# Performance work log

Measured on AMD Instinct MI355X. Metric: run time of the kernel, lower is better.

The kernel has to match this reference:

```python
import jax, jax.numpy as jnp
import numpy as np
from jax import lax

B, N, K = 8, 4096, 64
RATIO1, R1 = 0.5, 0.2
RATIO2, R2 = 0.25, 0.4
SA1_DIMS = [3, 32, 32, 64]
SA2_DIMS = [64 + 3, 64, 64, 128]
SA3_DIMS = [128 + 3, 128, 256, 512]


def _mlp_params(key, dims, prefix):
    params = {}
    for i, (din, dout) in enumerate(zip(dims[:-1], dims[1:])):
        key, k1 = jax.random.split(key)
        s = 1.0 / np.sqrt(din)
        params[f"{prefix}_w{i}"] = jax.random.uniform(k1, (din, dout), jnp.float32, -s, s)
        params[f"{prefix}_b{i}"] = jnp.zeros((dout,), jnp.float32)
    return params, key


def setup_inputs() -> dict:
    key = jax.random.key(0)
    key, kp = jax.random.split(key)
    inp = {"pos": jax.random.uniform(kp, (B, N, 3), jnp.float32)}  # unit-cube point clouds
    p1, key = _mlp_params(key, SA1_DIMS, "sa1"); inp.update(p1)
    p2, key = _mlp_params(key, SA2_DIMS, "sa2"); inp.update(p2)
    p3, key = _mlp_params(key, SA3_DIMS, "sa3"); inp.update(p3)
    key, k1, k2 = jax.random.split(key, 3)
    s = 1.0 / np.sqrt(512)
    inp["w_mu"] = jax.random.uniform(k1, (512, 32), jnp.float32, -s, s)
    inp["b_mu"] = jnp.zeros((32,), jnp.float32)
    inp["w_lv"] = jax.random.uniform(k2, (512, 32), jnp.float32, -s, s)
    inp["b_lv"] = jnp.zeros((32,), jnp.float32)
    return inp


def _mlp(x, params):
    # PyG MLP semantics (plain_last=True): ReLU on all but the final layer.
    for i, (w, b) in enumerate(params):
        x = x @ w + b
        if i < len(params) - 1:
            x = jax.nn.relu(x)
    return x


def _fps(pos, M):
    # Farthest point sampling, deterministic start at index 0. pos: [N,3] -> [M]
    n = pos.shape[0]
    def step(carry, _):
        dist, far = carry
        d = jnp.sum((pos - pos[far]) ** 2, axis=-1)
        dist = jnp.minimum(dist, d)
        return (dist, jnp.argmax(dist).astype(jnp.int32)), far
    _, idx = lax.scan(step, (jnp.full(n, jnp.inf, pos.dtype), jnp.int32(0)), None, length=M)
    return idx


def _sa(x, pos, ratio, r, params):
    # SAModule: FPS -> radius query (K nearest within r) -> gather -> MLP -> masked max
    Nn = pos.shape[1]
    M = int(round(ratio * Nn))
    idx = jax.vmap(lambda p: _fps(p, M))(pos)                 # [B,M]
    centers = jax.vmap(lambda p, i: p[i])(pos, idx)           # [B,M,3]
    d2 = jnp.sum((centers[:, :, None, :] - pos[:, None, :, :]) ** 2, axis=-1)  # [B,M,N]
    neg = jnp.where(d2 <= r * r, -d2, -jnp.inf)
    vals, nbr = lax.top_k(neg, K)                             # [B,M,K]
    mask = vals > -jnp.inf                                    # valid neighbors (self always valid)
    pos_j = jax.vmap(lambda p, i: p[i])(pos, nbr)             # [B,M,K,3]
    rel = pos_j - centers[:, :, None, :]
    if x is None:
        feat = rel
    else:
        x_j = jax.vmap(lambda f, i: f[i])(x, nbr)             # [B,M,K,C]
        feat = jnp.concatenate([x_j, rel], axis=-1)
    h = _mlp(feat, params)                                    # [B,M,K,C']
    h = jnp.where(mask[..., None], h, -jnp.inf)
    out = jnp.max(h, axis=2)                                  # scatter-max aggregation
    out = jnp.where(jnp.isfinite(out), out, 0.0)
    return out, centers


def reference(pos, sa1_w0, sa1_b0, sa1_w1, sa1_b1, sa1_w2, sa1_b2,
              sa2_w0, sa2_b0, sa2_w1, sa2_b1, sa2_w2, sa2_b2,
              sa3_w0, sa3_b0, sa3_w1, sa3_b1, sa3_w2, sa3_b2,
              w_mu, b_mu, w_lv, b_lv):
    p1 = [(sa1_w0, sa1_b0), (sa1_w1, sa1_b1), (sa1_w2, sa1_b2)]
    p2 = [(sa2_w0, sa2_b0), (sa2_w1, sa2_b1), (sa2_w2, sa2_b2)]
    p3 = [(sa3_w0, sa3_b0), (sa3_w1, sa3_b1), (sa3_w2, sa3_b2)]
    x1, pos1 = _sa(None, pos, RATIO1, R1, p1)                 # [B,2048,64]
    x2, pos2 = _sa(x1, pos1, RATIO2, R2, p2)                  # [B,512,128]
    g = _mlp(jnp.concatenate([x2, pos2], axis=-1), p3)        # [B,512,512]
    feat = jnp.max(g, axis=1)                                 # global max pool [B,512]
    mu = feat @ w_mu + b_mu
    log_var = feat @ w_lv + b_lv
    eps = jax.random.normal(jax.random.key(42), mu.shape, mu.dtype)
    z = mu + eps * jnp.exp(0.5 * log_var)
    return (z, mu, log_var)
```

## Files before the change

### kernel.cpp

```cpp
#include <hip/hip_runtime.h>
#include <cstdint>
#include <cstddef>


constexpr int BATCH = 8;
constexpr int NPT0  = 4096;
constexpr int M1    = 2048;
constexpr int M2    = 512;
constexpr int KNB   = 64;
constexpr int CAP   = 1024;
constexpr int NCONS = 248;

constexpr size_t O_WT1S1 = 0;
constexpr size_t O_WT2S1 = 96;
constexpr size_t O_WT3S1 = 1120;
constexpr size_t O_WT1S2 = 3168;
constexpr size_t O_WT2S2 = 7456;
constexpr size_t O_WT3S2 = 11552;
constexpr size_t O_WT1S3 = 19744;
constexpr size_t O_WT2S3 = 36512;
constexpr size_t O_POS1  = 69280;
constexpr size_t O_X1    = 134816;
constexpr size_t O_POS2  = 1183392;
constexpr size_t O_X2    = 1199776;
constexpr size_t O_PROG  = 1724064;
constexpr size_t O_POS4  = 1724080;
constexpr size_t O_H2G   = O_X1;
constexpr size_t O_FP    = O_X2;

template <int C>
__device__ __forceinline__ int dppmov(int x) {
  return __builtin_amdgcn_update_dpp(x, x, C, 0xF, 0xF, false);
}

__device__ __forceinline__ float wave_fmax_scal(float x) {
  x = fmaxf(x, __int_as_float(dppmov<0x111>(__float_as_int(x))));
  x = fmaxf(x, __int_as_float(dppmov<0x112>(__float_as_int(x))));
  x = fmaxf(x, __int_as_float(dppmov<0x114>(__float_as_int(x))));
  x = fmaxf(x, __int_as_float(dppmov<0x118>(__float_as_int(x))));
  x = fmaxf(x, __int_as_float(dppmov<0x142>(__float_as_int(x))));
  x = fmaxf(x, __int_as_float(dppmov<0x143>(__float_as_int(x))));
  return __int_as_float(__builtin_amdgcn_readlane(__float_as_int(x), 63));
}

template <int C>
__device__ __forceinline__ void dpp_key_max(uint32_t& lo, uint32_t& hi) {
  uint32_t olo = (uint32_t)dppmov<C>((int)lo);
  uint32_t ohi = (uint32_t)dppmov<C>((int)hi);
  bool bet = (ohi > hi) || (ohi == hi && olo > lo);
  lo = bet ? olo : lo;
  hi = bet ? ohi : hi;
}
__device__ __forceinline__ void wave_key_max_scal(uint32_t& lo, uint32_t& hi) {
  dpp_key_max<0x111>(lo, hi);
  dpp_key_max<0x112>(lo, hi);
  dpp_key_max<0x114>(lo, hi);
  dpp_key_max<0x118>(lo, hi);
  dpp_key_max<0x142>(lo, hi);
  dpp_key_max<0x143>(lo, hi);
  lo = (uint32_t)__builtin_amdgcn_readlane((int)lo, 63);
  hi = (uint32_t)__builtin_amdgcn_readlane((int)hi, 63);
}
template <int C>
__device__ __forceinline__ void dpp_key_min(uint32_t& lo, uint32_t& hi) {
  uint32_t olo = (uint32_t)dppmov<C>((int)lo);
  uint32_t ohi = (uint32_t)dppmov<C>((int)hi);
  bool bet = (ohi < hi) || (ohi == hi && olo < lo);
  lo = bet ? olo : lo;
  hi = bet ? ohi : hi;
}
__device__ __forceinline__ void wave_key_min_scal(uint32_t& lo, uint32_t& hi) {
  dpp_key_min<0x111>(lo, hi);
  dpp_key_min<0x112>(lo, hi);
  dpp_key_min<0x114>(lo, hi);
  dpp_key_min<0x118>(lo, hi);
  dpp_key_min<0x142>(lo, hi);
  dpp_key_min<0x143>(lo, hi);
  lo = (uint32_t)__builtin_amdgcn_readlane((int)lo, 63);
  hi = (uint32_t)__builtin_amdgcn_readlane((int)hi, 63);
}

__device__ __forceinline__ void wave_lds_fence() {
  asm volatile("s_waitcnt lgkmcnt(0)" ::: "memory");
}

__device__ __forceinline__ uint32_t rotl32(uint32_t x, int d) {
  return (x << d) | (x >> (32 - d));
}

__device__ __forceinline__ void threefry_0_42(uint32_t c0, uint32_t c1,
                                              uint32_t& o0, uint32_t& o1) {
  const uint32_t k0 = 0u, k1 = 42u;
  const uint32_t ks[3] = {k0, k1, k0 ^ k1 ^ 0x1BD11BDAu};
  uint32_t x0 = c0 + ks[0];
  uint32_t x1 = c1 + ks[1];
  const int R0[4] = {13, 15, 26, 6};
  const int R1[4] = {17, 29, 16, 24};
  #pragma unroll
  for (int g = 0; g < 5; ++g) {
    const int* R = (g & 1) ? R1 : R0;
    #pragma unroll
    for (int r = 0; r < 4; ++r) {
      x0 += x1;
      x1 = rotl32(x1, R[r]);
      x1 ^= x0;
    }
    x0 += ks[(g + 1) % 3];
    x1 += ks[(g + 2) % 3] + (uint32_t)(g + 1);
  }
  o0 = x0; o1 = x1;
}

__device__ __forceinline__ float erfinv_xla(float x) {
  float w = -log1pf(-x * x);
  float p;
  if (w < 5.0f) {
    w = w - 2.5f;
    p = 2.81022636e-08f;
    p = fmaf(p, w, 3.43273939e-07f);
    p = fmaf(p, w, -3.5233877e-06f);
    p = fmaf(p, w, -4.39150654e-06f);
    p = fmaf(p, w, 0.00021858087f);
    p = fmaf(p, w, -0.00125372503f);
    p = fmaf(p, w, -0.00417768164f);
    p = fmaf(p, w, 0.246640727f);
    p = fmaf(p, w, 1.50140941f);
  } else {
    w = sqrtf(w) - 3.0f;
    p = -0.000200214257f;
    p = fmaf(p, w, 0.000100950558f);
    p = fmaf(p, w, 0.00134934322f);
    p = fmaf(p, w, -0.00367342844f);
    p = fmaf(p, w, 0.00573950773f);
    p = fmaf(p, w, -0.0076224613f);
    p = fmaf(p, w, 0.00943887047f);
    p = fmaf(p, w, 1.00167406f);
    p = fmaf(p, w, 2.83297682f);
  }
  return p * x;
}

__global__ __launch_bounds__(256) void prep_transpose(
    const float* __restrict__ a0, const float* __restrict__ a1,
    const float* __restrict__ a2, const float* __restrict__ a3,
    const float* __restrict__ a4, const float* __restrict__ a5,
    const float* __restrict__ a6, const float* __restrict__ a7,
    const float* __restrict__ pos, float* __restrict__ ws) {
  int u0 = blockIdx.x * 256 + threadIdx.x;
  if (u0 < 16) ((int*)(ws + O_PROG))[u0] = 0;
  int u = u0;
  if (u < 96)    { ws[O_WT1S1 + u] = a0[(u % 3)   * 32  + u / 3];   return; } u -= 96;
  if (u < 1024)  { ws[O_WT2S1 + u] = a1[(u % 32)  * 32  + u / 32];  return; } u -= 1024;
  if (u < 2048)  { ws[O_WT3S1 + u] = a2[(u % 32)  * 64  + u / 32];  return; } u -= 2048;
  if (u < 4288)  { ws[O_WT1S2 + u] = a3[(u % 67)  * 64  + u / 67];  return; } u -= 4288;
  if (u < 4096)  { ws[O_WT2S2 + u] = a4[(u % 64)  * 64  + u / 64];  return; } u -= 4096;
  if (u < 8192)  { ws[O_WT3S2 + u] = a5[(u % 64)  * 128 + u / 64];  return; } u -= 8192;
  if (u < 16768) { ws[O_WT1S3 + u] = a6[(u % 131) * 128 + u / 131]; return; } u -= 16768;
  if (u < 32768) { ws[O_WT2S3 + u] = a7[(u % 128) * 256 + u / 128]; return; } u -= 32768;
  if (u < 32768) {
    float x = pos[u * 3 + 0], y = pos[u * 3 + 1], z = pos[u * 3 + 2];
    ((float4*)(ws + O_POS4))[u] = make_float4(x, y, z, 0.0f);
  }
}

template <int N, int M>
__device__ __forceinline__ void fps_body(const float* __restrict__ pos4,
                                         float* __restrict__ centers,
                                         int* __restrict__ prog,
                                         char* smem, int b) {
  constexpr int T   = 512;
  constexpr int PPT = N / T;
  float* px = (float*)smem;
  float* py = px + N;
  float* pz = py + N;
  int*   tags  = (int*)(pz + N);
  uint2* kslot = (uint2*)(tags + 16);
  const int tid  = threadIdx.x;
  const int lane = tid & 63;
  const int wid  = tid >> 6;
  const float4* pb4 = (const float4*)pos4 + (size_t)b * N;

  if (tid < 16) tags[tid] = -1;
  for (int i = tid; i < N; i += T) {
    float4 q = pb4[i];
    px[i] = q.x; py[i] = q.y; pz[i] = q.z;
  }
  __syncthreads();

  float mx[PPT], my[PPT], mz[PPT], md[PPT];
  #pragma unroll
  for (int s = 0; s < PPT; ++s) {
    int i = s * T + tid;
    mx[s] = px[i]; my[s] = py[i]; mz[s] = pz[i];
    md[s] = __builtin_inff();
  }

  float cx = px[0], cy = py[0], cz = pz[0];
  float* cb = centers + (size_t)b * M * 4;

  for (int m = 0; m < M; ++m) {
    if (tid == 0) {
      *(float4*)(cb + m * 4) = make_float4(cx, cy, cz, 0.0f);
      if ((m & 63) == 63)
        __hip_atomic_store(prog + b, m + 1, __ATOMIC_RELEASE,
                           __HIP_MEMORY_SCOPE_AGENT);
    }
    float bv = -1.0f;
    int   bi = 0x7FFFFFFF;
    {
      #pragma clang fp contract(off)
      #pragma unroll
      for (int s = 0; s < PPT; ++s) {
        float dx = mx[s] - cx, dy = my[s] - cy, dz = mz[s] - cz;
        float d = (dx * dx + dy * dy) + dz * dz;
        float nd = fminf(md[s], d);
        md[s] = nd;
        if (nd > bv) { bv = nd; bi = s * T + tid; }
      }
    }
    uint32_t klo = ~(uint32_t)bi;
    uint32_t khi = __float_as_uint(bv);
    dpp_key_max<0x111>(klo, khi);
    dpp_key_max<0x112>(klo, khi);
    dpp_key_max<0x114>(klo, khi);
    dpp_key_max<0x118>(klo, khi);

    const int par = (m & 1) * 32;
    if ((lane & 15) == 15)
      kslot[par + wid * 4 + (lane >> 4)] = make_uint2(klo, khi);
    __builtin_amdgcn_fence(__ATOMIC_RELEASE, "workgroup");
    if (lane == 63)
      __hip_atomic_store(&tags[wid], m, __ATOMIC_RELAXED,
                         __HIP_MEMORY_SCOPE_WORKGROUP);
    for (;;) {
      int t = __hip_atomic_load(&tags[lane & 7], __ATOMIC_RELAXED,
                                __HIP_MEMORY_SCOPE_WORKGROUP);
      if (__ballot(t >= m) == ~0ull) break;
    }
    __builtin_amdgcn_fence(__ATOMIC_ACQUIRE, "workgroup");

    uint2 kk = kslot[par + (lane & 31)];
    uint32_t K0 = kk.x, K1 = kk.y;
    wave_key_max_scal(K0, K1);
    int p = (int)~K0;
    cx = px[p]; cy = py[p]; cz = pz[p];
  }
}

template <int NPTS, int DF, int D1, int D2, int DOUT, int MM, int CH>
__device__ __forceinline__ void sa_body(
    const float* __restrict__ pts4, const float* __restrict__ feats,
    const float* __restrict__ centers, float* __restrict__ outf,
    const float* __restrict__ wt1, const float* __restrict__ bz1,
    const float* __restrict__ wt2, const float* __restrict__ bz2,
    const float* __restrict__ wt3, const float* __restrict__ bz3,
    float r2max, int* __restrict__ prog, char* smem) {
  constexpr int DIN = DF + 3;
  constexpr int NCHUNK = MM / CH;
  const int lane = threadIdx.x & 63;
  const int wid  = threadIdx.x >> 6;
  const int g0 = ((int)blockIdx.x - 8) * 8 + wid;
  const int b = g0 & 7;
  const int rank = g0 >> 3;
  float* sd = (float*)(smem + wid * 8192);
  int*   si = (int*)(smem + wid * 8192 + 4096);
  const float4* pb4 = (const float4*)pts4 + (size_t)b * NPTS;

  for (int chunk = rank; chunk < NCHUNK; chunk += NCONS) {
    const int m0 = chunk * CH;
    const int mlast = m0 + CH - 1;
    for (;;) {
      int r = 0;
      if (lane == 0)
        r = __hip_atomic_load(prog + b, __ATOMIC_RELAXED,
                              __HIP_MEMORY_SCOPE_AGENT);
      r = __builtin_amdgcn_readfirstlane(r);
      if (r > mlast) break;
      if (mlast - r > 128) __builtin_amdgcn_s_sleep(64);
      else                 __builtin_amdgcn_s_sleep(4);
    }
    __builtin_amdgcn_fence(__ATOMIC_ACQUIRE, "agent");

    for (int m = m0; m <= mlast; ++m) {
      const float* cc = centers + ((size_t)b * MM + m) * 4;
      const float cx = cc[0], cy = cc[1], cz = cc[2];

      int cnt = 0;
      const unsigned long long ltmask = (1ull << lane) - 1ull;
      for (int base = 0; base < NPTS; base += 64) {
        int i = base + lane;
        float4 q = pb4[i];
        float d2;
        {
          #pragma clang fp contract(off)
          float dx = cx - q.x, dy = cy - q.y, dz = cz - q.z;
          d2 = (dx * dx + dy * dy) + dz * dz;
        }
        bool inr = (d2 <= r2max);
        unsigned long long mk = __ballot(inr);
        int p = cnt + (int)__popcll(mk & ltmask);
        if (inr && p < CAP) { sd[p] = d2; si[p] = i; }
        cnt += (int)__popcll(mk);
      }
      if (cnt > CAP) cnt = CAP;
      wave_lds_fence();

      int my_nbr = -1;
      if (cnt <= KNB) {
        my_nbr = (lane < cnt) ? si[lane] : -1;
      } else {
        constexpr int SMAX = CAP / 64;
        float rd[SMAX];
        #pragma unroll
        for (int s = 0; s < SMAX; ++s) {
          rd[s] = __builtin_inff();
          if (s * 64 < cnt) {
            int q = s * 64 + lane;
            if (q < cnt) rd[s] = sd[q];
          }
        }
        for (int k = 0; k < KNB; ++k) {
          float bv = rd[0];
          int   bp = lane;
          #pragma unroll
          for (int s = 1; s < SMAX; ++s) {
            if (s * 64 < cnt) {
              if (rd[s] < bv) { bv = rd[s]; bp = s * 64 + lane; }
            }
          }
          uint32_t klo = (uint32_t)bp;
          uint32_t khi = __float_as_uint(bv);
          wave_key_min_scal(klo, khi);
          int bpw = (int)klo;
          if (lane == k) my_nbr = si[bpw];
          int wl = bpw & 63, wsl = bpw >> 6;
          #pragma unroll
          for (int s = 0; s < SMAX; ++s) {
            if (s * 64 < cnt) {
              rd[s] = (lane == wl && s == wsl) ? __builtin_inff() : rd[s];
            }
          }
        }
      }
      const bool valid = (my_nbr >= 0);
      const int safeN = valid ? my_nbr : 0;

      float rel[3];
      {
        float4 pr = pb4[safeN];
        rel[0] = pr.x - cx; rel[1] = pr.y - cy; rel[2] = pr.z - cz;
      }
      float xin[DF > 0 ? DF : 1];
      if constexpr (DF > 0) {
        const float* xr = feats + ((size_t)b * NPTS + safeN) * DF;
        #pragma unroll
        for (int i = 0; i < DF; i += 4) {
          float4 v = *reinterpret_cast<const float4*>(xr + i);
          xin[i] = v.x; xin[i + 1] = v.y; xin[i + 2] = v.z; xin[i + 3] = v.w;
        }
      }

      float h1[D1];
      for (int c = 0; c < D1; c += 4) {
        const float* w0 = wt1 + (c + 0) * DIN;
        const float* w1 = wt1 + (c + 1) * DIN;
        const float* w2 = wt1 + (c + 2) * DIN;
        const float* w3 = wt1 + (c + 3) * DIN;
        float a0 = bz1[c + 0], a1 = bz1[c + 1], a2 = bz1[c + 2], a3 = bz1[c + 3];
        if constexpr (DF > 0) {
          #pragma unroll
          for (int i = 0; i < DF; ++i) {
            a0 = fmaf(xin[i], w0[i], a0);
            a1 = fmaf(xin[i], w1[i], a1);
            a2 = fmaf(xin[i], w2[i], a2);
            a3 = fmaf(xin[i], w3[i], a3);
          }
        }
        #pragma unroll
        for (int r = 0; r < 3; ++r) {
          a0 = fmaf(rel[r], w0[DF + r], a0);
          a1 = fmaf(rel[r], w1[DF + r], a1);
          a2 = fmaf(rel[r], w2[DF + r], a2);
          a3 = fmaf(rel[r], w3[DF + r], a3);
        }
        h1[c + 0] = fmaxf(a0, 0.0f);
        h1[c + 1] = fmaxf(a1, 0.0f);
        h1[c + 2] = fmaxf(a2, 0.0f);
        h1[c + 3] = fmaxf(a3, 0.0f);
      }

      float h2[D2];
      for (int c = 0; c < D2; c += 4) {
        const float* w0 = wt2 + (c + 0) * D1;
        const float* w1 = wt2 + (c + 1) * D1;
        const float* w2 = wt2 + (c + 2) * D1;
        const float* w3 = wt2 + (c + 3) * D1;
        float a0 = bz2[c + 0], a1 = bz2[c + 1], a2 = bz2[c + 2], a3 = bz2[c + 3];
        #pragma unroll
        for (int i = 0; i < D1; ++i) {
          a0 = fmaf(h1[i], w0[i], a0);
          a1 = fmaf(h1[i], w1[i], a1);
          a2 = fmaf(h1[i], w2[i], a2);
          a3 = fmaf(h1[i], w3[i], a3);
        }
        h2[c + 0] = fmaxf(a0, 0.0f);
        h2[c + 1] = fmaxf(a1, 0.0f);
        h2[c + 2] = fmaxf(a2, 0.0f);
        h2[c + 3] = fmaxf(a3, 0.0f);
      }

      float* orow = outf + ((size_t)b * MM + m) * DOUT;
      #pragma unroll
      for (int u = 0; u < DOUT / 64; ++u) {
        float outv = 0.0f;
        for (int ccb = 0; ccb < 64; ccb += 4) {
          const int c = u * 64 + ccb;
          const float* w0 = wt3 + (c + 0) * D2;
          const float* w1 = wt3 + (c + 1) * D2;
          const float* w2 = wt3 + (c + 2) * D2;
          const float* w3 = wt3 + (c + 3) * D2;
          float a0 = bz3[c + 0], a1 = bz3[c + 1], a2 = bz3[c + 2], a3 = bz3[c + 3];
          #pragma unroll
          for (int i = 0; i < D2; ++i) {
            a0 = fmaf(h2[i], w0[i], a0);
            a1 = fmaf(h2[i], w1[i], a1);
            a2 = fmaf(h2[i], w2[i], a2);
            a3 = fmaf(h2[i], w3[i], a3);
          }
          const float NI = -__builtin_inff();
          float s0 = wave_fmax_scal(valid ? a0 : NI);
          float s1 = wave_fmax_scal(valid ? a1 : NI);
          float s2 = wave_fmax_scal(valid ? a2 : NI);
          float s3 = wave_fmax_scal(valid ? a3 : NI);
          if (lane == ccb + 0) outv = s0;
          if (lane == ccb + 1) outv = s1;
          if (lane == ccb + 2) outv = s2;
          if (lane == ccb + 3) outv = s3;
        }
        orow[u * 64 + lane] = outv;
      }
    }
  }
}

__global__ __launch_bounds__(512, 2) void stageA_kernel(
    float* __restrict__ ws,
    const float* __restrict__ bz1, const float* __restrict__ bz2,
    const float* __restrict__ bz3) {
  extern __shared__ char smem[];
  int* prog = (int*)(ws + O_PROG);
  if (blockIdx.x < 8) {
    asm volatile("s_setprio 3");
    fps_body<NPT0, M1>(ws + O_POS4, ws + O_POS1, prog, smem, blockIdx.x);
  } else {
    sa_body<NPT0, 0, 32, 32, 64, M1, 8>(
        ws + O_POS4, nullptr, ws + O_POS1, ws + O_X1,
        ws + O_WT1S1, bz1, ws + O_WT2S1, bz2, ws + O_WT3S1, bz3,
        0.04f, prog, smem);
  }
}

__global__ __launch_bounds__(512, 2) void stageB_kernel(
    float* __restrict__ ws,
    const float* __restrict__ bz1, const float* __restrict__ bz2,
    const float* __restrict__ bz3) {
  extern __shared__ char smem[];
  int* prog = (int*)(ws + O_PROG) + 8;
  if (blockIdx.x < 8) {
    asm volatile("s_setprio 3");
    fps_body<M1, M2>(ws + O_POS1, ws + O_POS2, prog, smem, blockIdx.x);
  } else {
    sa_body<M1, 64, 64, 64, 128, M2, 2>(
        ws + O_POS1, ws + O_X1, ws + O_POS2, ws + O_X2,
        ws + O_WT1S2, bz1, ws + O_WT2S2, bz2, ws + O_WT3S2, bz3,
        0.16f, prog, smem);
  }
}

__global__ __launch_bounds__(256) void sa3_l12_kernel(
    const float* __restrict__ x2, const float* __restrict__ pos2,
    const float* __restrict__ wt1, const float* __restrict__ bz1,
    const float* __restrict__ wt2, const float* __restrict__ bz2,
    float* __restrict__ h2g) {
  __shared__ float H[64 * 132];
  const int tid = threadIdx.x;
  const int lane = tid & 63, w = tid >> 6;
  const int b = blockIdx.x >> 3, tile = blockIdx.x & 7;
  const int pt = tile * 64 + lane;
  const float* xrow = x2 + ((size_t)b * 512 + pt) * 128;
  float* hrow = H + lane * 132;
  const int c0 = w * 32;

  float f[64];
  #pragma unroll
  for (int i = 0; i < 64; i += 4) {
    float4 v = *reinterpret_cast<const float4*>(xrow + i);
    f[i] = v.x; f[i + 1] = v.y; f[i + 2] = v.z; f[i + 3] = v.w;
  }
  for (int c = c0; c < c0 + 32; ++c) {
    const float* wv = wt1 + c * 131;
    float acc = bz1[c];
    #pragma unroll
    for (int i = 0; i < 64; ++i) acc = fmaf(f[i], wv[i], acc);
    hrow[c] = acc;
  }
  #pragma unroll
  for (int i = 0; i < 64; i += 4) {
    float4 v = *reinterpret_cast<const float4*>(xrow + 64 + i);
    f[i] = v.x; f[i + 1] = v.y; f[i + 2] = v.z; f[i + 3] = v.w;
  }
  float q0, q1, q2;
  {
    const float* pr = pos2 + ((size_t)b * 512 + pt) * 4;
    q0 = pr[0]; q1 = pr[1]; q2 = pr[2];
  }
  for (int c = c0; c < c0 + 32; ++c) {
    const float* wv = wt1 + c * 131 + 64;
    float acc = hrow[c];
    #pragma unroll
    for (int i = 0; i < 64; ++i) acc = fmaf(f[i], wv[i], acc);
    acc = fmaf(q0, wv[64], acc);
    acc = fmaf(q1, wv[65], acc);
    acc = fmaf(q2, wv[66], acc);
    hrow[c] = fmaxf(acc, 0.0f);
  }
  __syncthreads();

  float h[128];
  #pragma unroll
  for (int i = 0; i < 128; i += 4) {
    float4 v = *reinterpret_cast<const float4*>(hrow + i);
    h[i] = v.x; h[i + 1] = v.y; h[i + 2] = v.z; h[i + 3] = v.w;
  }
  float* grow = h2g + ((size_t)b * 512 + pt) * 256;
  const int c1 = w * 64;
  for (int c = c1; c < c1 + 64; ++c) {
    const float* wv = wt2 + c * 128;
    float acc = bz2[c];
    #pragma unroll
    for (int i = 0; i < 128; ++i) acc = fmaf(h[i], wv[i], acc);
    grow[c] = fmaxf(acc, 0.0f);
  }
}

__global__ __launch_bounds__(256) void sa3_l3_kernel(
    const float* __restrict__ h2g, const float* __restrict__ w3,
    const float* __restrict__ bz3, float* __restrict__ fpart) {
  const int tid = threadIdx.x;
  const int blk = blockIdx.x;
  const int b   = blk >> 6;
  const int t16 = (blk >> 1) & 31;
  const int cb  = blk & 1;
  const int c = cb * 256 + tid;
  const float* hbase = h2g + ((size_t)b * 512 + t16 * 16) * 256;

  float acc[16];
  #pragma unroll
  for (int j = 0; j < 16; ++j) acc[j] = 0.0f;

  for (int i0 = 0; i0 < 256; i0 += 8) {
    float wv[8];
    #pragma unroll
    for (int u = 0; u < 8; ++u) wv[u] = w3[(size_t)(i0 + u) * 512 + c];
    #pragma unroll
    for (int j = 0; j < 16; ++j) {
      const float* hr = hbase + (size_t)j * 256 + i0;
      #pragma unroll
      for (int u = 0; u < 8; ++u) acc[j] = fmaf(hr[u], wv[u], acc[j]);
    }
  }
  float mv = acc[0];
  #pragma unroll
  for (int j = 1; j < 16; ++j) mv = fmaxf(mv, acc[j]);
  fpart[((size_t)b * 32 + t16) * 512 + c] = mv + bz3[c];
}

__global__ __launch_bounds__(64) void final_kernel(
    const float* __restrict__ fpart,
    const float* __restrict__ wmu, const float* __restrict__ bmu,
    const float* __restrict__ wlv, const float* __restrict__ blv,
    float* __restrict__ outp) {
  __shared__ float feat[512];
  const int tid = threadIdx.x;
  const int b = blockIdx.x;
  for (int cidx = tid; cidx < 512; cidx += 64) {
    float mv = fpart[(size_t)b * 32 * 512 + cidx];
    #pragma unroll
    for (int t = 1; t < 32; ++t)
      mv = fmaxf(mv, fpart[((size_t)b * 32 + t) * 512 + cidx]);
    feat[cidx] = mv;
  }
  __syncthreads();
  if (tid < 32) {
    const int c = tid;
    double amu = 0.0, alv = 0.0;
    for (int i = 0; i < 512; ++i) {
      double fv = (double)feat[i];
      amu += fv * (double)wmu[i * 32 + c];
      alv += fv * (double)wlv[i * 32 + c];
    }
    float mu = (float)amu + bmu[c];
    float lv = (float)alv + blv[c];

    uint32_t n = (uint32_t)(b * 32 + c);
    uint32_t o0, o1;
    threefry_0_42(0u, n, o0, o1);
    uint32_t bits = o0 ^ o1;
    float fl = __uint_as_float((bits >> 9) | 0x3f800000u) - 1.0f;
    const float LO = -0.99999994039535522461f;
    float u = fl * 2.0f + LO;
    u = fmaxf(LO, u);
    float eps = 1.4142135623730951f * erfinv_xla(u);
    float z = mu + eps * expf(0.5f * lv);

    outp[b * 32 + c] = z;
    outp[256 + b * 32 + c] = mu;
    outp[512 + b * 32 + c] = lv;
  }
}

extern "C" void kernel_launch(void* const* d_in, const int* in_sizes, int n_in,
                              void* d_out, int out_size, void* d_ws, size_t ws_size,
                              hipStream_t stream) {
  (void)in_sizes; (void)n_in; (void)out_size; (void)ws_size;
  const float* pos  = (const float*)d_in[0];
  const float* s1w0 = (const float*)d_in[1];  const float* s1b0 = (const float*)d_in[2];
  const float* s1w1 = (const float*)d_in[3];  const float* s1b1 = (const float*)d_in[4];
  const float* s1w2 = (const float*)d_in[5];  const float* s1b2 = (const float*)d_in[6];
  const float* s2w0 = (const float*)d_in[7];  const float* s2b0 = (const float*)d_in[8];
  const float* s2w1 = (const float*)d_in[9];  const float* s2b1 = (const float*)d_in[10];
  const float* s2w2 = (const float*)d_in[11]; const float* s2b2 = (const float*)d_in[12];
  const float* s3w0 = (const float*)d_in[13]; const float* s3b0 = (const float*)d_in[14];
  const float* s3w1 = (const float*)d_in[15]; const float* s3b1 = (const float*)d_in[16];
  const float* s3w2 = (const float*)d_in[17]; const float* s3b2 = (const float*)d_in[18];
  const float* wmu  = (const float*)d_in[19]; const float* bmu  = (const float*)d_in[20];
  const float* wlv  = (const float*)d_in[21]; const float* blv  = (const float*)d_in[22];
  float* ws = (float*)d_ws;
  float* out = (float*)d_out;

  prep_transpose<<<399, 256, 0, stream>>>(s1w0, s1w1, s1w2, s2w0, s2w1, s2w2,
                                          s3w0, s3w1, pos, ws);

  stageA_kernel<<<8 + NCONS, 512, 65536, stream>>>(ws, s1b0, s1b1, s1b2);

  stageB_kernel<<<8 + NCONS, 512, 65536, stream>>>(ws, s2b0, s2b1, s2b2);

  sa3_l12_kernel<<<BATCH * 8, 256, 0, stream>>>(
      ws + O_X2, ws + O_POS2, ws + O_WT1S3, s3b0, ws + O_WT2S3, s3b1,
      ws + O_H2G);

  sa3_l3_kernel<<<BATCH * 64, 256, 0, stream>>>(ws + O_H2G, s3w2, s3b2,
                                                ws + O_FP);

  final_kernel<<<BATCH, 64, 0, stream>>>(ws + O_FP, wmu, bmu, wlv, blv, out);
}
```

Before: 3.912 ms.

## Run farthest point sampling in a single wavefront to drop cross-wave sync

The farthest point sampling loop now runs on one 64-lane wavefront instead of eight. Points are kept as float4 in shared memory and re-read each iteration, and the argmax is a single wave reduction, so the per-iteration tag spin-wait and cross-wave key exchange go away. The cost is eight times more distance work per lane plus repeated LDS loads on a serial critical path. The stage A and B kernels also request 80 KB of dynamic shared memory when the attribute call succeeds, which may lower occupancy for the consumer blocks.

```diff
diff --git a/kernel.cpp b/kernel.cpp
--- a/kernel.cpp
+++ b/kernel.cpp
@@ -168,38 +168,26 @@
                                          float* __restrict__ centers,
                                          int* __restrict__ prog,
                                          char* smem, int b) {
-  constexpr int T   = 512;
-  constexpr int PPT = N / T;
-  float* px = (float*)smem;
-  float* py = px + N;
-  float* pz = py + N;
-  int*   tags  = (int*)(pz + N);
-  uint2* kslot = (uint2*)(tags + 16);
+  constexpr int PPL = N / 64;
+  float4* ps = (float4*)smem;
   const int tid  = threadIdx.x;
   const int lane = tid & 63;
-  const int wid  = tid >> 6;
   const float4* pb4 = (const float4*)pos4 + (size_t)b * N;
 
-  if (tid < 16) tags[tid] = -1;
-  for (int i = tid; i < N; i += T) {
-    float4 q = pb4[i];
-    px[i] = q.x; py[i] = q.y; pz[i] = q.z;
-  }
+  for (int i = tid; i < N; i += 512) ps[i] = pb4[i];
   __syncthreads();
-
-  float mx[PPT], my[PPT], mz[PPT], md[PPT];
+  if (tid >= 64) return;
+
+  float md[PPL];
   #pragma unroll
-  for (int s = 0; s < PPT; ++s) {
-    int i = s * T + tid;
-    mx[s] = px[i]; my[s] = py[i]; mz[s] = pz[i];
-    md[s] = __builtin_inff();
-  }
-
-  float cx = px[0], cy = py[0], cz = pz[0];
+  for (int s = 0; s < PPL; ++s) md[s] = __builtin_inff();
+
+  float4 c0 = ps[0];
+  float cx = c0.x, cy = c0.y, cz = c0.z;
   float* cb = centers + (size_t)b * M * 4;
 
   for (int m = 0; m < M; ++m) {
-    if (tid == 0) {
+    if (lane == 0) {
       *(float4*)(cb + m * 4) = make_float4(cx, cy, cz, 0.0f);
       if ((m & 63) == 63)
         __hip_atomic_store(prog + b, m + 1, __ATOMIC_RELEASE,
@@ -210,40 +198,22 @@
     {
       #pragma clang fp contract(off)
       #pragma unroll
-      for (int s = 0; s < PPT; ++s) {
-        float dx = mx[s] - cx, dy = my[s] - cy, dz = mz[s] - cz;
+      for (int s = 0; s < PPL; ++s) {
+        float4 q = ps[s * 64 + lane];
+        float dx = q.x - cx, dy = q.y - cy, dz = q.z - cz;
         float d = (dx * dx + dy * dy) + dz * dz;
         float nd = fminf(md[s], d);
         md[s] = nd;
-        if (nd > bv) { bv = nd; bi = s * T + tid; }
+        if (nd > bv) { bv = nd; bi = s * 64 + lane; }
       }
     }
     uint32_t klo = ~(uint32_t)bi;
     uint32_t khi = __float_as_uint(bv);
-    dpp_key_max<0x111>(klo, khi);
-    dpp_key_max<0x112>(klo, khi);
-    dpp_key_max<0x114>(klo, khi);
-    dpp_key_max<0x118>(klo, khi);
-
-    const int par = (m & 1) * 32;
-    if ((lane & 15) == 15)
-      kslot[par + wid * 4 + (lane >> 4)] = make_uint2(klo, khi);
-    __builtin_amdgcn_fence(__ATOMIC_RELEASE, "workgroup");
-    if (lane == 63)
-      __hip_atomic_store(&tags[wid], m, __ATOMIC_RELAXED,
-                         __HIP_MEMORY_SCOPE_WORKGROUP);
-    for (;;) {
-      int t = __hip_atomic_load(&tags[lane & 7], __ATOMIC_RELAXED,
-                                __HIP_MEMORY_SCOPE_WORKGROUP);
-      if (__ballot(t >= m) == ~0ull) break;
-    }
-    __builtin_amdgcn_fence(__ATOMIC_ACQUIRE, "workgroup");
-
-    uint2 kk = kslot[par + (lane & 31)];
-    uint32_t K0 = kk.x, K1 = kk.y;
-    wave_key_max_scal(K0, K1);
-    int p = (int)~K0;
-    cx = px[p]; cy = py[p]; cz = pz[p];
+    wave_key_max_scal(klo, khi);
+    int p = (int)~klo;
+
+    float4 w = ps[p];
+    cx = w.x; cy = w.y; cz = w.z;
   }
 }
 
@@ -638,12 +608,20 @@
   float* ws = (float*)d_ws;
   float* out = (float*)d_out;
 
+  int smemA = 81920, smemB = 81920;
+  if (hipFuncSetAttribute((const void*)stageA_kernel,
+                          hipFuncAttributeMaxDynamicSharedMemorySize,
+                          81920) != hipSuccess) smemA = 65536;
+  if (hipFuncSetAttribute((const void*)stageB_kernel,
+                          hipFuncAttributeMaxDynamicSharedMemorySize,
+                          81920) != hipSuccess) smemB = 65536;
+
   prep_transpose<<<399, 256, 0, stream>>>(s1w0, s1w1, s1w2, s2w0, s2w1, s2w2,
                                           s3w0, s3w1, pos, ws);
 
-  stageA_kernel<<<8 + NCONS, 512, 65536, stream>>>(ws, s1b0, s1b1, s1b2);
-
-  stageB_kernel<<<8 + NCONS, 512, 65536, stream>>>(ws, s2b0, s2b1, s2b2);
+  stageA_kernel<<<8 + NCONS, 512, smemA, stream>>>(ws, s1b0, s1b1, s1b2);
+
+  stageB_kernel<<<8 + NCONS, 512, smemB, stream>>>(ws, s2b0, s2b1, s2b2);
 
   sa3_l12_kernel<<<BATCH * 8, 256, 0, stream>>>(
       ws + O_X2, ws + O_POS2, ws + O_WT1S3, s3b0, ws + O_WT2S3, s3b1,
```

After: 7.289 ms. 86.3% more time.
